# Performance work log

Measured on AMD Instinct MI355X. Metric: run time of the kernel, lower is better.

The kernel has to match this reference:

```python
import jax, jax.numpy as jnp
import numpy as np

N = 262144          # flattened tokens (batch * seq)
D = 256             # bert_hidden_units
C = 50001           # num_items + 1


def setup_inputs() -> dict:
    key = jax.random.key(0)
    k1, k2, k3, k4 = jax.random.split(key, 4)
    inputs_row = jax.random.normal(k1, (N, D), dtype=jnp.float32)
    center = jax.random.normal(k2, (C, D), dtype=jnp.float32)
    target_row = jax.random.randint(k3, (N,), 0, C, dtype=jnp.int64)
    target = jax.random.randint(k4, (4096,), 0, C, dtype=jnp.int64)
    return {"inputs_row": inputs_row, "center": center,
            "target_row": target_row, "target": target}


def reference(inputs_row, center, target_row, target):
    # Fused scatter-mean replacement of the per-class Python loop:
    # for i in unique(target): center[i] = mean(inputs_row[target_row == i])
    num_classes = center.shape[0]
    sums = jax.ops.segment_sum(inputs_row, target_row, num_segments=num_classes)          # [C, D]
    counts = jax.ops.segment_sum(jnp.ones((inputs_row.shape[0],), inputs_row.dtype),
                                 target_row, num_segments=num_classes)                   # [C]
    mean = sums / jnp.where(counts > 0, counts, 1.0)[:, None]                            # [C, D]
    # only classes appearing in `target` are considered, and only those with
    # a nonzero row_mask (counts > 0) actually overwrite center[i]
    present = jnp.zeros((num_classes,), dtype=bool).at[target].set(True)
    upd = present & (counts > 0)
    return jnp.where(upd[:, None], mean, center)
```

## Files before the change

kernel.cpp:

```cpp
#include <hip/hip_runtime.h>

#define N_TOK 262144
#define DDIM  256
#define CCLS  50001
#define ROW4  (DDIM / 4)
#define NBLK  2048
#define NTHR  256
#define ROWS_PER_BLK (N_TOK / NBLK)
#define TOTAL4 ((long long)CCLS * ROW4)
#define SLAB   ((TOTAL4 + NBLK - 1) / NBLK)

typedef __attribute__((ext_vector_type(4))) float f4;

__global__ __launch_bounds__(NTHR)
void build_copy_kernel(const int* __restrict__ trow,
                       int* __restrict__ heads,
                       int* __restrict__ next,
                       const float* __restrict__ center,
                       float* __restrict__ out) {
    const int tid = threadIdx.x;

    if (tid < ROWS_PER_BLK) {
        const int i = blockIdx.x * ROWS_PER_BLK + tid;
        const int t = trow[i];
        const int old = atomicExch(&heads[t], i + 1);
        next[i] = old;
    }

    const long long base = (long long)blockIdx.x * SLAB;
    long long end = base + SLAB;
    if (end > TOTAL4) end = TOTAL4;
    const f4* __restrict__ src = reinterpret_cast<const f4*>(center);
    f4* __restrict__ dst = reinterpret_cast<f4*>(out);
    for (long long j = base + tid; j < end; j += NTHR) {
        f4 v = __builtin_nontemporal_load(&src[j]);
        __builtin_nontemporal_store(v, &dst[j]);
    }
}

__global__ void update_kernel(const float* __restrict__ in,
                              const int* __restrict__ tgt, int n_tgt,
                              const int* __restrict__ heads,
                              const int* __restrict__ next,
                              float* __restrict__ out) {
    const int wid  = threadIdx.x >> 6;
    const int lane = threadIdx.x & 63;
    const int i = blockIdx.x * 4 + wid;
    if (i >= n_tgt) return;

    const int c = tgt[i];
    int r = heads[c];
    if (r == 0) return;

    float4 acc = {0.f, 0.f, 0.f, 0.f};
    int cnt = 0;
    while (r != 0) {
        const int row = r - 1;
        const float4 v =
            reinterpret_cast<const float4*>(in)[(long long)row * ROW4 + lane];
        r = next[row];
        acc.x += v.x; acc.y += v.y; acc.z += v.z; acc.w += v.w;
        ++cnt;
    }
    const float s = 1.0f / (float)cnt;
    float4 m = {acc.x * s, acc.y * s, acc.z * s, acc.w * s};
    reinterpret_cast<float4*>(out)[(long long)c * ROW4 + lane] = m;
}

extern "C" void kernel_launch(void* const* d_in, const int* in_sizes, int n_in,
                              void* d_out, int out_size, void* d_ws, size_t ws_size,
                              hipStream_t stream) {
    const float* inputs_row = (const float*)d_in[0];
    const float* center     = (const float*)d_in[1];
    const int*   target_row = (const int*)d_in[2];
    const int*   target     = (const int*)d_in[3];
    const int    n_target   = in_sizes[3];

    float* out = (float*)d_out;

    int* heads = (int*)d_ws;
    int* next  = heads + CCLS;

    hipMemsetAsync(heads, 0, (size_t)CCLS * sizeof(int), stream);

    build_copy_kernel<<<NBLK, NTHR, 0, stream>>>(target_row, heads, next, center, out);

    update_kernel<<<(n_target + 3) / 4, 256, 0, stream>>>(inputs_row, target, n_target,
                                                          heads, next, out);
}
```

Before: 50.28 us.

## Split center copy into separate merge pass using compact mean buffer and slot map

Removes the center-to-output copy from the linked-list build kernel. The gather kernel now writes per-target means into a compact buffer indexed by target slot, and a new merge kernel writes every output row from either the mean buffer or center, chosen by a slot map. The build kernel switches to one token per thread. This adds a third launch and an extra memset region. The full-output copy now runs after the gather instead of alongside the atomic list build.

After: 50.41 us. About the same (+0.3%).

```diff
diff --git a/kernel.cpp b/kernel.cpp
--- a/kernel.cpp
+++ b/kernel.cpp
@@ -4,48 +4,30 @@
 #define DDIM  256
 #define CCLS  50001
 #define ROW4  (DDIM / 4)
-#define NBLK  2048
-#define NTHR  256
-#define ROWS_PER_BLK (N_TOK / NBLK)
-#define TOTAL4 ((long long)CCLS * ROW4)
-#define SLAB   ((TOTAL4 + NBLK - 1) / NBLK)
+#define TOTAL4 (CCLS * ROW4)
 
-typedef __attribute__((ext_vector_type(4))) float f4;
-
-__global__ __launch_bounds__(NTHR)
-void build_copy_kernel(const int* __restrict__ trow,
-                       int* __restrict__ heads,
-                       int* __restrict__ next,
-                       const float* __restrict__ center,
-                       float* __restrict__ out) {
-    const int tid = threadIdx.x;
-
-    if (tid < ROWS_PER_BLK) {
-        const int i = blockIdx.x * ROWS_PER_BLK + tid;
+__global__ void build_kernel(const int* __restrict__ trow,
+                             const int* __restrict__ tgt, int n_tgt,
+                             int* __restrict__ heads,
+                             int* __restrict__ next,
+                             int* __restrict__ slotmap) {
+    const int i = blockIdx.x * blockDim.x + threadIdx.x;
+    if (i < N_TOK) {
         const int t = trow[i];
         const int old = atomicExch(&heads[t], i + 1);
         next[i] = old;
     }
-
-    const long long base = (long long)blockIdx.x * SLAB;
-    long long end = base + SLAB;
-    if (end > TOTAL4) end = TOTAL4;
-    const f4* __restrict__ src = reinterpret_cast<const f4*>(center);
-    f4* __restrict__ dst = reinterpret_cast<f4*>(out);
-    for (long long j = base + tid; j < end; j += NTHR) {
-        f4 v = __builtin_nontemporal_load(&src[j]);
-        __builtin_nontemporal_store(v, &dst[j]);
-    }
+    if (i < n_tgt) slotmap[tgt[i]] = i + 1;
 }
 
-__global__ void update_kernel(const float* __restrict__ in,
-                              const int* __restrict__ tgt, int n_tgt,
-                              const int* __restrict__ heads,
-                              const int* __restrict__ next,
-                              float* __restrict__ out) {
-    const int wid  = threadIdx.x >> 6;
+__global__ __launch_bounds__(256)
+void gather_kernel(const float* __restrict__ in,
+                   const int* __restrict__ tgt, int n_tgt,
+                   const int* __restrict__ heads,
+                   const int* __restrict__ next,
+                   float* __restrict__ mean_buf) {
     const int lane = threadIdx.x & 63;
-    const int i = blockIdx.x * 4 + wid;
+    const int i = (blockIdx.x * 256 + threadIdx.x) >> 6;
     if (i >= n_tgt) return;
 
     const int c = tgt[i];
@@ -64,7 +46,25 @@
     }
     const float s = 1.0f / (float)cnt;
     float4 m = {acc.x * s, acc.y * s, acc.z * s, acc.w * s};
-    reinterpret_cast<float4*>(out)[(long long)c * ROW4 + lane] = m;
+    reinterpret_cast<float4*>(mean_buf)[(long long)i * ROW4 + lane] = m;
+}
+
+__global__ __launch_bounds__(256)
+void merge_kernel(const float4* __restrict__ center,
+                  const float4* __restrict__ mean_buf,
+                  const int* __restrict__ heads,
+                  const int* __restrict__ slotmap,
+                  float4* __restrict__ out) {
+    const int j = blockIdx.x * 256 + threadIdx.x;
+    if (j >= TOTAL4) return;
+    const int r = j >> 6;
+    const int o = j & 63;
+    const int s = slotmap[r];
+    const bool upd = (s > 0) && (heads[r] != 0);
+    const float4* __restrict__ src =
+        upd ? mean_buf + (long long)(s - 1) * ROW4
+            : center + (long long)r * ROW4;
+    out[j] = src[o];
 }
 
 extern "C" void kernel_launch(void* const* d_in, const int* in_sizes, int n_in,
@@ -78,13 +78,22 @@
 
     float* out = (float*)d_out;
 
-    int* heads = (int*)d_ws;
-    int* next  = heads + CCLS;
+    int* heads    = (int*)d_ws;
+    int* slotmap  = heads + CCLS;
+    int* next     = slotmap + CCLS;
+    float* mean_buf = (float*)(next + N_TOK);
 
-    hipMemsetAsync(heads, 0, (size_t)CCLS * sizeof(int), stream);
+    hipMemsetAsync(heads, 0, (size_t)2 * CCLS * sizeof(int), stream);
 
-    build_copy_kernel<<<NBLK, NTHR, 0, stream>>>(target_row, heads, next, center, out);
+    build_kernel<<<(N_TOK + 255) / 256, 256, 0, stream>>>(target_row, target,
+                                                          n_target, heads, next,
+                                                          slotmap);
 
-    update_kernel<<<(n_target + 3) / 4, 256, 0, stream>>>(inputs_row, target, n_target,
-                                                          heads, next, out);
+    gather_kernel<<<(n_target * 64 + 255) / 256, 256, 0, stream>>>(
+        inputs_row, target, n_target, heads, next, mean_buf);
+
+    merge_kernel<<<(TOTAL4 + 255) / 256, 256, 0, stream>>>(
+        reinterpret_cast<const float4*>(center),
+        reinterpret_cast<const float4*>(mean_buf),
+        heads, slotmap, reinterpret_cast<float4*>(out));
 }
```
